# Performance work log

Hardware: AMD Instinct MI355X
Metric: run time of the kernel (lower is better)

## Reference

```python
import jax, jax.numpy as jnp
from jax import lax
import numpy as np

B, T, F, H = 1024, 512, 1, 60


def _p(key, shape, scale):
    return jax.random.uniform(key, shape, jnp.float32, -scale, scale)


def setup_inputs() -> dict:
    key = jax.random.key(0)
    ks = jax.random.split(key, 40)
    s = 1.0 / np.sqrt(H)
    d = {
        "inputs": jax.random.normal(ks[0], (B, T, F), jnp.float32),
        "outputs": jax.random.normal(ks[1], (B, T, F), jnp.float32),
        # encoder GRU: 3 layers, PyTorch layout W_ih [3H, in], W_hh [3H, H]
        "eW_ih0": _p(ks[2], (3 * H, F), s), "eW_hh0": _p(ks[3], (3 * H, H), s),
        "eb_ih0": _p(ks[4], (3 * H,), s), "eb_hh0": _p(ks[5], (3 * H,), s),
        "eW_ih1": _p(ks[6], (3 * H, H), s), "eW_hh1": _p(ks[7], (3 * H, H), s),
        "eb_ih1": _p(ks[8], (3 * H,), s), "eb_hh1": _p(ks[9], (3 * H,), s),
        "eW_ih2": _p(ks[10], (3 * H, H), s), "eW_hh2": _p(ks[11], (3 * H, H), s),
        "eb_ih2": _p(ks[12], (3 * H,), s), "eb_hh2": _p(ks[13], (3 * H,), s),
        # decoder GRUCells
        "c1_Wih": _p(ks[14], (3 * H, F), s), "c1_Whh": _p(ks[15], (3 * H, H), s),
        "c1_bih": _p(ks[16], (3 * H,), s), "c1_bhh": _p(ks[17], (3 * H,), s),
        "c2_Wih": _p(ks[18], (3 * H, H), s), "c2_Whh": _p(ks[19], (3 * H, H), s),
        "c2_bih": _p(ks[20], (3 * H,), s), "c2_bhh": _p(ks[21], (3 * H,), s),
        "c3_Wih": _p(ks[22], (3 * H, H), s), "c3_Whh": _p(ks[23], (3 * H, H), s),
        "c3_bih": _p(ks[24], (3 * H,), s), "c3_bhh": _p(ks[25], (3 * H,), s),
        # output linear
        "lin_W": _p(ks[26], (F, H), s), "lin_b": _p(ks[27], (F,), s),
    }
    return d


def gru_step(x, h, Wih, Whh, bih, bhh):
    # PyTorch GRU gate math
    gi = x @ Wih.T + bih  # [B, 3H]
    gh = h @ Whh.T + bhh
    ir, iz, inn = jnp.split(gi, 3, axis=-1)
    hr, hz, hn = jnp.split(gh, 3, axis=-1)
    r = jax.nn.sigmoid(ir + hr)
    z = jax.nn.sigmoid(iz + hz)
    n = jnp.tanh(inn + r * hn)
    return (1.0 - z) * n + z * h


def run_gru_layer(x_tbf, Wih, Whh, bih, bhh):
    h0 = jnp.zeros((x_tbf.shape[1], H), x_tbf.dtype)

    def step(h, xt):
        h2 = gru_step(xt, h, Wih, Whh, bih, bhh)
        return h2, h2

    hT, ys = lax.scan(step, h0, x_tbf)
    return ys, hT


def reference(inputs, outputs,
              eW_ih0, eW_hh0, eb_ih0, eb_hh0,
              eW_ih1, eW_hh1, eb_ih1, eb_hh1,
              eW_ih2, eW_hh2, eb_ih2, eb_hh2,
              c1_Wih, c1_Whh, c1_bih, c1_bhh,
              c2_Wih, c2_Whh, c2_bih, c2_bhh,
              c3_Wih, c3_Whh, c3_bih, c3_bhh,
              lin_W, lin_b):
    # --- encoder: 3-layer GRU (eval mode -> inter-layer dropout is identity)
    x = jnp.swapaxes(inputs, 0, 1)  # [T, B, F]
    ys0, h0T = run_gru_layer(x, eW_ih0, eW_hh0, eb_ih0, eb_hh0)
    ys1, h1T = run_gru_layer(ys0, eW_ih1, eW_hh1, eb_ih1, eb_hh1)
    _, h2T = run_gru_layer(ys1, eW_ih2, eW_hh2, eb_ih2, eb_hh2)
    encoded_vec = jnp.stack([h0T, h1T, h2T])  # [3, B, H]

    # --- decoder: 3 stacked GRUCells per step (dropout identity in eval)
    outs_r = jnp.swapaxes(outputs, 0, 1)  # [T, B, F]
    carry0 = (encoded_vec[2], encoded_vec[1], encoded_vec[0])

    def dec_step(carry, xt):
        h1, h2, h3 = carry
        h1 = gru_step(xt, h1, c1_Wih, c1_Whh, c1_bih, c1_bhh)
        h2 = gru_step(h1, h2, c2_Wih, c2_Whh, c2_bih, c2_bhh)
        h3 = gru_step(h2, h3, c3_Wih, c3_Whh, c3_bih, c3_bhh)
        pred = h3 @ lin_W.T + lin_b  # [B, F]
        return (h1, h2, h3), pred

    _, preds = lax.scan(dec_step, carry0, outs_r)  # [T, B, F]
    predicted = jnp.swapaxes(preds, 0, 1)  # [B, T, F]
    return predicted, jnp.swapaxes(encoded_vec, 0, 1)  # [B, 3, H]
```

## Files before the change

### kernel.cpp

```cpp
#include <hip/hip_runtime.h>
#include <hip/hip_bf16.h>

namespace {

constexpr int B = 1024, T = 512, H = 60, G = 180, NTHR = 192;
constexpr int TT = 8;
constexpr int NT = T / TT;

__device__ __forceinline__ float sigm(float x) { return 1.f / (1.f + __expf(-x)); }
__device__ __forceinline__ float tanh_fast(float x) {
  x = fminf(fmaxf(x, -15.f), 15.f);
  const float e = __expf(-2.f * x);
  return (1.f - e) / (1.f + e);
}

__device__ __forceinline__ float ldcvt(const float* p) { return *p; }
__device__ __forceinline__ float ldcvt(const __hip_bfloat16* p) { return __bfloat162float(*p); }
__device__ __forceinline__ void stcvt(float* p, float v) { *p = v; }
__device__ __forceinline__ void stcvt(__hip_bfloat16* p, float v) { *p = __float2bfloat16(v); }

#define ACCH(i, dst)                                                  \
  {                                                                   \
    const float4 hv = *(const float4*)&h_sh[(i) * 4];                 \
    dst = fmaf(Wh##i.x, hv.x, dst);                                   \
    dst = fmaf(Wh##i.y, hv.y, dst);                                   \
    dst = fmaf(Wh##i.z, hv.z, dst);                                   \
    dst = fmaf(Wh##i.w, hv.w, dst);                                   \
  }
#define ACCH_ALL                                                      \
  ACCH(0, c0) ACCH(1, c1) ACCH(2, c2) ACCH(3, c3)                     \
  ACCH(4, c0) ACCH(5, c1) ACCH(6, c2) ACCH(7, c3)                     \
  ACCH(8, c0) ACCH(9, c1) ACCH(10, c2) ACCH(11, c3)                   \
  ACCH(12, c0) ACCH(13, c1) ACCH(14, c2)

#define LWH_ALL                                                       \
  LWH(0) LWH(1) LWH(2) LWH(3) LWH(4) LWH(5) LWH(6) LWH(7)             \
  LWH(8) LWH(9) LWH(10) LWH(11) LWH(12) LWH(13) LWH(14)

template <typename TS, bool WRITE_YS, bool WRITE_ENC>
__global__ __launch_bounds__(NTHR, 1) void gru_scalar_kernel(
    const float* __restrict__ xscalar,
    const float* __restrict__ Wih,
    const float* __restrict__ Whh,
    const float* __restrict__ bih, const float* __restrict__ bhh,
    const float* __restrict__ h_init,
    TS* __restrict__ ys_out,
    float* __restrict__ enc_out)
{
  const int tid = threadIdx.x;
  const int b = blockIdx.x;

  __shared__ __align__(16) float h_sh[64];
  __shared__ float Ar[60], Az[60], Nn[60], Hn[60];
  __shared__ float xs_seq[T];

  const int rr = (tid < G) ? tid : 0;

  float4 Wh0, Wh1, Wh2, Wh3, Wh4, Wh5, Wh6, Wh7, Wh8, Wh9, Wh10, Wh11, Wh12, Wh13, Wh14;
#define LWH(i) Wh##i = *(const float4*)&Whh[(size_t)rr * H + (i) * 4];
  LWH_ALL
#undef LWH
  const float wih0 = Wih[rr];
  const float bi = bih[rr];
  const float bh = bhh[rr];

  if (tid < H) h_sh[tid] = h_init ? h_init[(size_t)b * G + tid] : 0.f;
  for (int i = tid; i < T; i += NTHR) xs_seq[i] = xscalar[(size_t)b * T + i];
  __syncthreads();

  const int g = tid / H;
  const int j = tid - g * H;

  for (int t = 0; t < T; ++t) {
    if (tid < G) {
      float c0 = bh, c1 = 0.f, c2 = 0.f, c3 = 0.f;
      ACCH_ALL
      const float c = (c0 + c1) + (c2 + c3);
      const float a = fmaf(wih0, xs_seq[t], bi);
      if (g == 0)       Ar[j] = a + c;
      else if (g == 1)  Az[j] = a + c;
      else            { Nn[j] = a; Hn[j] = c; }
    }
    __syncthreads();

    if (tid < H) {
      const float rg = sigm(Ar[tid]);
      const float zg = sigm(Az[tid]);
      const float nv = tanh_fast(fmaf(rg, Hn[tid], Nn[tid]));
      const float hnew = fmaf(zg, h_sh[tid] - nv, nv);
      h_sh[tid] = hnew;
      if constexpr (WRITE_YS)
        stcvt(&ys_out[(size_t)t * B * H + (size_t)b * H + tid], hnew);
    }
    __syncthreads();
  }

  if constexpr (WRITE_ENC) {
    if (tid < H) enc_out[(size_t)b * G + tid] = h_sh[tid];
  }
}

template <typename TS, bool WRITE_YS, bool WRITE_ENC, bool WRITE_PRED>
__global__ __launch_bounds__(NTHR, 1) void gru_vec_kernel(
    const TS* __restrict__ xseq,
    const float* __restrict__ Wih,
    const float* __restrict__ Whh,
    const float* __restrict__ bih, const float* __restrict__ bhh,
    const float* __restrict__ h_init,
    TS* __restrict__ ys_out,
    float* __restrict__ enc_out,
    float* __restrict__ pred_out,
    const float* __restrict__ lin_W,
    const float* __restrict__ lin_b)
{
  const int tid = threadIdx.x;
  const int b = blockIdx.x;

  __shared__ __align__(16) float h_sh[64];
  __shared__ __align__(16) float x_sh[2][TT * H];
  __shared__ float gi_sh[TT][G];
  __shared__ float Ar[60], Az[60], Nn[60], Hn[60];
  __shared__ float pv[64];

  const int rr = (tid < G) ? tid : 0;

  float4 Wh0, Wh1, Wh2, Wh3, Wh4, Wh5, Wh6, Wh7, Wh8, Wh9, Wh10, Wh11, Wh12, Wh13, Wh14;
#define LWH(i) Wh##i = *(const float4*)&Whh[(size_t)rr * H + (i) * 4];
  LWH_ALL
#undef LWH
  const float bi = bih[rr];
  const float bh = bhh[rr];

  float linw = 0.f, linb = 0.f;
  if constexpr (WRITE_PRED) {
    linw = lin_W[tid < H ? tid : 0];
    linb = lin_b[0];
  }

  if (tid < H) h_sh[tid] = h_init ? h_init[(size_t)b * G + tid] : 0.f;

  {
    const int i0 = tid, i1 = tid + NTHR, i2 = tid + 2 * NTHR;
    {
      const int s = i0 / H, hh = i0 - s * H;
      x_sh[0][i0] = ldcvt(&xseq[((size_t)s * B + b) * H + hh]);
    }
    {
      const int s = i1 / H, hh = i1 - s * H;
      x_sh[0][i1] = ldcvt(&xseq[((size_t)s * B + b) * H + hh]);
    }
    if (i2 < TT * H) {
      const int s = i2 / H, hh = i2 - s * H;
      x_sh[0][i2] = ldcvt(&xseq[((size_t)s * B + b) * H + hh]);
    }
  }
  __syncthreads();

  const int g = tid / H;
  const int j = tid - g * H;

  for (int tile = 0; tile < NT; ++tile) {
    const int cur = tile & 1;

    float xr0 = 0.f, xr1 = 0.f, xr2 = 0.f;
    const int i0 = tid, i1 = tid + NTHR, i2 = tid + 2 * NTHR;
    if (tile + 1 < NT) {
      const size_t tb = (size_t)(tile + 1) * TT;
      {
        const int s = i0 / H, hh = i0 - s * H;
        xr0 = ldcvt(&xseq[((tb + s) * B + b) * H + hh]);
      }
      {
        const int s = i1 / H, hh = i1 - s * H;
        xr1 = ldcvt(&xseq[((tb + s) * B + b) * H + hh]);
      }
      if (i2 < TT * H) {
        const int s = i2 / H, hh = i2 - s * H;
        xr2 = ldcvt(&xseq[((tb + s) * B + b) * H + hh]);
      }
    }

    asm volatile("" ::: "memory");

    if (tid < G) {
      float acc[TT];
#pragma unroll
      for (int s = 0; s < TT; ++s) acc[s] = bi;
#pragma unroll
      for (int k = 0; k < H / 4; ++k) {
        const float4 w = *(const float4*)&Wih[(size_t)rr * H + k * 4];
#pragma unroll
        for (int s = 0; s < TT; ++s) {
          const float4 xv = *(const float4*)&x_sh[cur][s * H + k * 4];
          acc[s] = fmaf(w.x, xv.x, acc[s]);
          acc[s] = fmaf(w.y, xv.y, acc[s]);
          acc[s] = fmaf(w.z, xv.z, acc[s]);
          acc[s] = fmaf(w.w, xv.w, acc[s]);
        }
      }
#pragma unroll
      for (int s = 0; s < TT; ++s) gi_sh[s][rr] = acc[s];
    }

    if (tile + 1 < NT) {
      x_sh[cur ^ 1][i0] = xr0;
      x_sh[cur ^ 1][i1] = xr1;
      if (i2 < TT * H) x_sh[cur ^ 1][i2] = xr2;
    }
    __syncthreads();

    for (int s = 0; s < TT; ++s) {
      const int t = tile * TT + s;
      if (tid < G) {
        float c0 = bh, c1 = 0.f, c2 = 0.f, c3 = 0.f;
        ACCH_ALL
        const float c = (c0 + c1) + (c2 + c3);
        const float a = gi_sh[s][rr];
        if (g == 0)       Ar[j] = a + c;
        else if (g == 1)  Az[j] = a + c;
        else            { Nn[j] = a; Hn[j] = c; }
      }
      __syncthreads();

      if (tid < H) {
        const float rg = sigm(Ar[tid]);
        const float zg = sigm(Az[tid]);
        const float nv = tanh_fast(fmaf(rg, Hn[tid], Nn[tid]));
        const float hnew = fmaf(zg, h_sh[tid] - nv, nv);
        h_sh[tid] = hnew;
        if constexpr (WRITE_YS)
          stcvt(&ys_out[(size_t)t * B * H + (size_t)b * H + tid], hnew);
        if constexpr (WRITE_PRED) pv[tid] = hnew * linw;
      }
      __syncthreads();

      if constexpr (WRITE_PRED) {
        if (tid < 64) {
          float v = (tid < H) ? pv[tid] : 0.f;
#pragma unroll
          for (int off = 32; off; off >>= 1) v += __shfl_xor(v, off);
          if (tid == 0) pred_out[(size_t)b * T + t] = v + linb;
        }
      }
    }
  }

  if constexpr (WRITE_ENC) {
    if (tid < H) enc_out[(size_t)b * G + tid] = h_sh[tid];
  }
}

template <typename TS>
void launch_all(const float* inputs, const float* outputs,
                const float* eW_ih0, const float* eW_hh0, const float* eb_ih0, const float* eb_hh0,
                const float* eW_ih1, const float* eW_hh1, const float* eb_ih1, const float* eb_hh1,
                const float* eW_ih2, const float* eW_hh2, const float* eb_ih2, const float* eb_hh2,
                const float* c1_Wih, const float* c1_Whh, const float* c1_bih, const float* c1_bhh,
                const float* c2_Wih, const float* c2_Whh, const float* c2_bih, const float* c2_bhh,
                const float* c3_Wih, const float* c3_Whh, const float* c3_bih, const float* c3_bhh,
                const float* lin_W, const float* lin_b,
                float* pred, float* enc, void* d_ws, hipStream_t stream) {
  const size_t seq = (size_t)T * B * H;
  TS* ws0 = (TS*)d_ws;
  TS* ws1 = ws0 + seq;
  const dim3 grid(B), blk(NTHR);

  gru_scalar_kernel<TS, true, true><<<grid, blk, 0, stream>>>(
      inputs, eW_ih0, eW_hh0, eb_ih0, eb_hh0, nullptr, ws0, enc + 0);
  gru_vec_kernel<TS, true, true, false><<<grid, blk, 0, stream>>>(
      ws0, eW_ih1, eW_hh1, eb_ih1, eb_hh1, nullptr,
      ws1, enc + 60, nullptr, nullptr, nullptr);
  gru_vec_kernel<TS, false, true, false><<<grid, blk, 0, stream>>>(
      ws1, eW_ih2, eW_hh2, eb_ih2, eb_hh2, nullptr,
      nullptr, enc + 120, nullptr, nullptr, nullptr);
  gru_scalar_kernel<TS, true, false><<<grid, blk, 0, stream>>>(
      outputs, c1_Wih, c1_Whh, c1_bih, c1_bhh, enc + 120, ws0, nullptr);
  gru_vec_kernel<TS, true, false, false><<<grid, blk, 0, stream>>>(
      ws0, c2_Wih, c2_Whh, c2_bih, c2_bhh, enc + 60,
      ws1, nullptr, nullptr, nullptr, nullptr);
  gru_vec_kernel<TS, false, false, true><<<grid, blk, 0, stream>>>(
      ws1, c3_Wih, c3_Whh, c3_bih, c3_bhh, enc + 0,
      nullptr, nullptr, pred, lin_W, lin_b);
}

}

extern "C" void kernel_launch(void* const* d_in, const int* in_sizes, int n_in,
                              void* d_out, int out_size, void* d_ws, size_t ws_size,
                              hipStream_t stream) {
  const float* inputs  = (const float*)d_in[0];
  const float* outputs = (const float*)d_in[1];
  const float* eW_ih0 = (const float*)d_in[2];  const float* eW_hh0 = (const float*)d_in[3];
  const float* eb_ih0 = (const float*)d_in[4];  const float* eb_hh0 = (const float*)d_in[5];
  const float* eW_ih1 = (const float*)d_in[6];  const float* eW_hh1 = (const float*)d_in[7];
  const float* eb_ih1 = (const float*)d_in[8];  const float* eb_hh1 = (const float*)d_in[9];
  const float* eW_ih2 = (const float*)d_in[10]; const float* eW_hh2 = (const float*)d_in[11];
  const float* eb_ih2 = (const float*)d_in[12]; const float* eb_hh2 = (const float*)d_in[13];
  const float* c1_Wih = (const float*)d_in[14]; const float* c1_Whh = (const float*)d_in[15];
  const float* c1_bih = (const float*)d_in[16]; const float* c1_bhh = (const float*)d_in[17];
  const float* c2_Wih = (const float*)d_in[18]; const float* c2_Whh = (const float*)d_in[19];
  const float* c2_bih = (const float*)d_in[20]; const float* c2_bhh = (const float*)d_in[21];
  const float* c3_Wih = (const float*)d_in[22]; const float* c3_Whh = (const float*)d_in[23];
  const float* c3_bih = (const float*)d_in[24]; const float* c3_bhh = (const float*)d_in[25];
  const float* lin_W  = (const float*)d_in[26]; const float* lin_b  = (const float*)d_in[27];

  float* pred = (float*)d_out;
  float* enc  = pred + (size_t)B * T;

  const size_t seq = (size_t)T * B * H;

#define ARGS inputs, outputs, \
    eW_ih0, eW_hh0, eb_ih0, eb_hh0, eW_ih1, eW_hh1, eb_ih1, eb_hh1, \
    eW_ih2, eW_hh2, eb_ih2, eb_hh2, \
    c1_Wih, c1_Whh, c1_bih, c1_bhh, c2_Wih, c2_Whh, c2_bih, c2_bhh, \
    c3_Wih, c3_Whh, c3_bih, c3_bhh, lin_W, lin_b, pred, enc, d_ws, stream

  if (ws_size >= 2 * seq * sizeof(float)) {
    launch_all<float>(ARGS);
  } else {
    launch_all<__hip_bfloat16>(ARGS);
  }
#undef ARGS
}
```

Measured before the change: 3.467 ms.

## Split input projection into separate GEMM kernel, chunk recurrence over time

The input-to-hidden projection for the vector GRU layers moves out of the recurrent kernel into a standalone gi_gemm kernel that computes gate pre-activations for a chunk of timesteps. The recurrent kernel then only does the hidden matvec and prefetches precomputed gi values four steps ahead. The sequence is processed in chunks sized to the workspace. The bf16 fallback is dropped and ys is overwritten in place. The aim is to take the Wih matvec off the serial critical path, at the cost of extra global traffic for gi and more kernel launches.

```diff
diff --git a/kernel.cpp b/kernel.cpp
--- a/kernel.cpp
+++ b/kernel.cpp
@@ -4,8 +4,6 @@
 namespace {
 
 constexpr int B = 1024, T = 512, H = 60, G = 180, NTHR = 192;
-constexpr int TT = 8;
-constexpr int NT = T / TT;
 
 __device__ __forceinline__ float sigm(float x) { return 1.f / (1.f + __expf(-x)); }
 __device__ __forceinline__ float tanh_fast(float x) {
@@ -13,11 +11,6 @@
   const float e = __expf(-2.f * x);
   return (1.f - e) / (1.f + e);
 }
-
-__device__ __forceinline__ float ldcvt(const float* p) { return *p; }
-__device__ __forceinline__ float ldcvt(const __hip_bfloat16* p) { return __bfloat162float(*p); }
-__device__ __forceinline__ void stcvt(float* p, float v) { *p = v; }
-__device__ __forceinline__ void stcvt(__hip_bfloat16* p, float v) { *p = __float2bfloat16(v); }
 
 #define ACCH(i, dst)                                                  \
   {                                                                   \
@@ -27,24 +20,15 @@
     dst = fmaf(Wh##i.z, hv.z, dst);                                   \
     dst = fmaf(Wh##i.w, hv.w, dst);                                   \
   }
-#define ACCH_ALL                                                      \
-  ACCH(0, c0) ACCH(1, c1) ACCH(2, c2) ACCH(3, c3)                     \
-  ACCH(4, c0) ACCH(5, c1) ACCH(6, c2) ACCH(7, c3)                     \
-  ACCH(8, c0) ACCH(9, c1) ACCH(10, c2) ACCH(11, c3)                   \
-  ACCH(12, c0) ACCH(13, c1) ACCH(14, c2)
-
-#define LWH_ALL                                                       \
-  LWH(0) LWH(1) LWH(2) LWH(3) LWH(4) LWH(5) LWH(6) LWH(7)             \
-  LWH(8) LWH(9) LWH(10) LWH(11) LWH(12) LWH(13) LWH(14)
-
-template <typename TS, bool WRITE_YS, bool WRITE_ENC>
+
+template <bool WRITE_YS, bool WRITE_ENC>
 __global__ __launch_bounds__(NTHR, 1) void gru_scalar_kernel(
     const float* __restrict__ xscalar,
     const float* __restrict__ Wih,
     const float* __restrict__ Whh,
     const float* __restrict__ bih, const float* __restrict__ bhh,
     const float* __restrict__ h_init,
-    TS* __restrict__ ys_out,
+    float* __restrict__ ys_out,
     float* __restrict__ enc_out)
 {
   const int tid = threadIdx.x;
@@ -58,13 +42,15 @@
 
   float4 Wh0, Wh1, Wh2, Wh3, Wh4, Wh5, Wh6, Wh7, Wh8, Wh9, Wh10, Wh11, Wh12, Wh13, Wh14;
 #define LWH(i) Wh##i = *(const float4*)&Whh[(size_t)rr * H + (i) * 4];
-  LWH_ALL
+  LWH(0) LWH(1) LWH(2) LWH(3) LWH(4) LWH(5) LWH(6) LWH(7)
+  LWH(8) LWH(9) LWH(10) LWH(11) LWH(12) LWH(13) LWH(14)
 #undef LWH
   const float wih0 = Wih[rr];
   const float bi = bih[rr];
   const float bh = bhh[rr];
 
   if (tid < H) h_sh[tid] = h_init ? h_init[(size_t)b * G + tid] : 0.f;
+  if (tid >= H && tid < 64) h_sh[tid] = 0.f;
   for (int i = tid; i < T; i += NTHR) xs_seq[i] = xscalar[(size_t)b * T + i];
   __syncthreads();
 
@@ -74,7 +60,10 @@
   for (int t = 0; t < T; ++t) {
     if (tid < G) {
       float c0 = bh, c1 = 0.f, c2 = 0.f, c3 = 0.f;
-      ACCH_ALL
+      ACCH(0, c0) ACCH(1, c1) ACCH(2, c2) ACCH(3, c3)
+      ACCH(4, c0) ACCH(5, c1) ACCH(6, c2) ACCH(7, c3)
+      ACCH(8, c0) ACCH(9, c1) ACCH(10, c2) ACCH(11, c3)
+      ACCH(12, c0) ACCH(13, c1) ACCH(14, c2)
       const float c = (c0 + c1) + (c2 + c3);
       const float a = fmaf(wih0, xs_seq[t], bi);
       if (g == 0)       Ar[j] = a + c;
@@ -90,7 +79,7 @@
       const float hnew = fmaf(zg, h_sh[tid] - nv, nv);
       h_sh[tid] = hnew;
       if constexpr (WRITE_YS)
-        stcvt(&ys_out[(size_t)t * B * H + (size_t)b * H + tid], hnew);
+        ys_out[(size_t)t * B * H + (size_t)b * H + tid] = hnew;
     }
     __syncthreads();
   }
@@ -100,25 +89,88 @@
   }
 }
 
-template <typename TS, bool WRITE_YS, bool WRITE_ENC, bool WRITE_PRED>
-__global__ __launch_bounds__(NTHR, 1) void gru_vec_kernel(
-    const TS* __restrict__ xseq,
+__global__ __launch_bounds__(NTHR, 1) void gi_gemm_kernel(
+    const float* __restrict__ x,
     const float* __restrict__ Wih,
-    const float* __restrict__ Whh,
-    const float* __restrict__ bih, const float* __restrict__ bhh,
-    const float* __restrict__ h_init,
-    TS* __restrict__ ys_out,
+    const float* __restrict__ bih,
+    float* __restrict__ gi)
+{
+  __shared__ __align__(16) float xs[16 * 60];
+  const int tid = threadIdx.x;
+  const size_t row0 = (size_t)blockIdx.x * 16;
+  const int rr = (tid < G) ? tid : 0;
+
+  float4 W0, W1, W2, W3, W4, W5, W6, W7, W8, W9, W10, W11, W12, W13, W14;
+#define LW(i) W##i = *(const float4*)&Wih[(size_t)rr * H + (i) * 4];
+  LW(0) LW(1) LW(2) LW(3) LW(4) LW(5) LW(6) LW(7)
+  LW(8) LW(9) LW(10) LW(11) LW(12) LW(13) LW(14)
+#undef LW
+  const float bi = bih[rr];
+
+  {
+    const float4* s4 = (const float4*)(x + row0 * H);
+    float4* d4 = (float4*)xs;
+    d4[tid] = s4[tid];
+    const int i2 = tid + NTHR;
+    if (i2 < 240) d4[i2] = s4[i2];
+  }
+  __syncthreads();
+
+#define GX(s, a)                                                      \
+  {                                                                   \
+    const float4 xv = *(const float4*)&xb[(s) * H + 4 * kk];          \
+    a = fmaf(w.x, xv.x, a); a = fmaf(w.y, xv.y, a);                   \
+    a = fmaf(w.z, xv.z, a); a = fmaf(w.w, xv.w, a);                   \
+  }
+#define PASS(p)                                                       \
+  {                                                                   \
+    const float* xb = xs + (p) * 8 * H;                               \
+    float a0 = bi, a1 = bi, a2 = bi, a3 = bi;                         \
+    float a4 = bi, a5 = bi, a6 = bi, a7 = bi;                         \
+    _Pragma("unroll")                                                 \
+    for (int kk = 0; kk < 15; ++kk) {                                 \
+      float4 w;                                                       \
+      switch (kk) {                                                   \
+        case 0: w = W0; break;   case 1: w = W1; break;               \
+        case 2: w = W2; break;   case 3: w = W3; break;               \
+        case 4: w = W4; break;   case 5: w = W5; break;               \
+        case 6: w = W6; break;   case 7: w = W7; break;               \
+        case 8: w = W8; break;   case 9: w = W9; break;               \
+        case 10: w = W10; break; case 11: w = W11; break;             \
+        case 12: w = W12; break; case 13: w = W13; break;             \
+        default: w = W14; break;                                      \
+      }                                                               \
+      GX(0, a0) GX(1, a1) GX(2, a2) GX(3, a3)                         \
+      GX(4, a4) GX(5, a5) GX(6, a6) GX(7, a7)                         \
+    }                                                                 \
+    if (tid < G) {                                                    \
+      float* o = gi + (row0 + (p) * 8) * G + rr;                      \
+      o[0 * G] = a0; o[1 * G] = a1; o[2 * G] = a2; o[3 * G] = a3;     \
+      o[4 * G] = a4; o[5 * G] = a5; o[6 * G] = a6; o[7 * G] = a7;     \
+    }                                                                 \
+  }
+  PASS(0)
+  PASS(1)
+#undef PASS
+#undef GX
+}
+
+template <bool WRITE_YS, bool WRITE_PRED>
+__global__ __launch_bounds__(NTHR, 1) void gru_rec_kernel(
+    const float* __restrict__ gi,
+    const float* __restrict__ Whh, const float* __restrict__ bhh,
+    const float* __restrict__ h_in, int h_in_stride,
+    float* __restrict__ ys_out,
+    float* __restrict__ h_out,
     float* __restrict__ enc_out,
     float* __restrict__ pred_out,
-    const float* __restrict__ lin_W,
-    const float* __restrict__ lin_b)
+    const float* __restrict__ linW, const float* __restrict__ linb,
+    int t0, int nsteps)
 {
   const int tid = threadIdx.x;
   const int b = blockIdx.x;
 
   __shared__ __align__(16) float h_sh[64];
-  __shared__ __align__(16) float x_sh[2][TT * H];
-  __shared__ float gi_sh[TT][G];
   __shared__ float Ar[60], Az[60], Nn[60], Hn[60];
   __shared__ float pv[64];
 
@@ -126,161 +178,100 @@
 
   float4 Wh0, Wh1, Wh2, Wh3, Wh4, Wh5, Wh6, Wh7, Wh8, Wh9, Wh10, Wh11, Wh12, Wh13, Wh14;
 #define LWH(i) Wh##i = *(const float4*)&Whh[(size_t)rr * H + (i) * 4];
-  LWH_ALL
+  LWH(0) LWH(1) LWH(2) LWH(3) LWH(4) LWH(5) LWH(6) LWH(7)
+  LWH(8) LWH(9) LWH(10) LWH(11) LWH(12) LWH(13) LWH(14)
 #undef LWH
-  const float bi = bih[rr];
   const float bh = bhh[rr];
 
-  float linw = 0.f, linb = 0.f;
+  float linw = 0.f, lb = 0.f;
   if constexpr (WRITE_PRED) {
-    linw = lin_W[tid < H ? tid : 0];
-    linb = lin_b[0];
-  }
-
-  if (tid < H) h_sh[tid] = h_init ? h_init[(size_t)b * G + tid] : 0.f;
-
-  {
-    const int i0 = tid, i1 = tid + NTHR, i2 = tid + 2 * NTHR;
-    {
-      const int s = i0 / H, hh = i0 - s * H;
-      x_sh[0][i0] = ldcvt(&xseq[((size_t)s * B + b) * H + hh]);
-    }
-    {
-      const int s = i1 / H, hh = i1 - s * H;
-      x_sh[0][i1] = ldcvt(&xseq[((size_t)s * B + b) * H + hh]);
-    }
-    if (i2 < TT * H) {
-      const int s = i2 / H, hh = i2 - s * H;
-      x_sh[0][i2] = ldcvt(&xseq[((size_t)s * B + b) * H + hh]);
-    }
-  }
+    linw = linW[tid < H ? tid : 0];
+    lb = linb[0];
+  }
+
+  if (tid < H) h_sh[tid] = h_in ? h_in[(size_t)b * h_in_stride + tid] : 0.f;
+  if (tid >= H && tid < 64) h_sh[tid] = 0.f;
   __syncthreads();
 
-  const int g = tid / H;
-  const int j = tid - g * H;
-
-  for (int tile = 0; tile < NT; ++tile) {
-    const int cur = tile & 1;
-
-    float xr0 = 0.f, xr1 = 0.f, xr2 = 0.f;
-    const int i0 = tid, i1 = tid + NTHR, i2 = tid + 2 * NTHR;
-    if (tile + 1 < NT) {
-      const size_t tb = (size_t)(tile + 1) * TT;
-      {
-        const int s = i0 / H, hh = i0 - s * H;
-        xr0 = ldcvt(&xseq[((tb + s) * B + b) * H + hh]);
+  const int g = rr / H;
+  const int j = rr - g * H;
+  const bool rowact = tid < G;
+
+  float g0 = 0.f, g1 = 0.f, g2 = 0.f, g3 = 0.f;
+  if (rowact) {
+    g0 = gi[((size_t)0 * B + b) * G + rr];
+    g1 = gi[((size_t)1 * B + b) * G + rr];
+    g2 = gi[((size_t)2 * B + b) * G + rr];
+    g3 = gi[((size_t)3 * B + b) * G + rr];
+  }
+
+  for (int s = 0; s < nsteps; ++s) {
+    float gn = 0.f;
+    if (rowact && s + 4 < nsteps) gn = gi[((size_t)(s + 4) * B + b) * G + rr];
+
+    if (rowact) {
+      float c0 = bh, c1 = 0.f, c2 = 0.f, c3 = 0.f;
+      ACCH(0, c0) ACCH(1, c1) ACCH(2, c2) ACCH(3, c3)
+      ACCH(4, c0) ACCH(5, c1) ACCH(6, c2) ACCH(7, c3)
+      ACCH(8, c0) ACCH(9, c1) ACCH(10, c2) ACCH(11, c3)
+      ACCH(12, c0) ACCH(13, c1) ACCH(14, c2)
+      const float c = (c0 + c1) + (c2 + c3);
+      const float a = g0;
+      if (g == 0)       Ar[j] = a + c;
+      else if (g == 1)  Az[j] = a + c;
+      else            { Nn[j] = a; Hn[j] = c; }
+    }
+    g0 = g1; g1 = g2; g2 = g3; g3 = gn;
+    __syncthreads();
+
+    if (tid < H) {
+      const float rg = sigm(Ar[tid]);
+      const float zg = sigm(Az[tid]);
+      const float nv = tanh_fast(fmaf(rg, Hn[tid], Nn[tid]));
+      const float hnew = fmaf(zg, h_sh[tid] - nv, nv);
+      h_sh[tid] = hnew;
+      if constexpr (WRITE_YS)
+        ys_out[(size_t)s * B * H + (size_t)b * H + tid] = hnew;
+      if constexpr (WRITE_PRED) pv[tid] = hnew * linw;
+    }
+    __syncthreads();
+
+    if constexpr (WRITE_PRED) {
+      if (tid < 64) {
+        float v = (tid < H) ? pv[tid] : 0.f;
+#pragma unroll
+        for (int o = 32; o; o >>= 1) v += __shfl_xor(v, o);
+        if (tid == 0) pred_out[(size_t)b * T + t0 + s] = v + lb;
       }
-      {
-        const int s = i1 / H, hh = i1 - s * H;
-        xr1 = ldcvt(&xseq[((tb + s) * B + b) * H + hh]);
-      }
-      if (i2 < TT * H) {
-        const int s = i2 / H, hh = i2 - s * H;
-        xr2 = ldcvt(&xseq[((tb + s) * B + b) * H + hh]);
-      }
-    }
-
-    asm volatile("" ::: "memory");
-
-    if (tid < G) {
-      float acc[TT];
-#pragma unroll
-      for (int s = 0; s < TT; ++s) acc[s] = bi;
-#pragma unroll
-      for (int k = 0; k < H / 4; ++k) {
-        const float4 w = *(const float4*)&Wih[(size_t)rr * H + k * 4];
-#pragma unroll
-        for (int s = 0; s < TT; ++s) {
-          const float4 xv = *(const float4*)&x_sh[cur][s * H + k * 4];
-          acc[s] = fmaf(w.x, xv.x, acc[s]);
-          acc[s] = fmaf(w.y, xv.y, acc[s]);
-          acc[s] = fmaf(w.z, xv.z, acc[s]);
-          acc[s] = fmaf(w.w, xv.w, acc[s]);
-        }
-      }
-#pragma unroll
-      for (int s = 0; s < TT; ++s) gi_sh[s][rr] = acc[s];
-    }
-
-    if (tile + 1 < NT) {
-      x_sh[cur ^ 1][i0] = xr0;
-      x_sh[cur ^ 1][i1] = xr1;
-      if (i2 < TT * H) x_sh[cur ^ 1][i2] = xr2;
-    }
-    __syncthreads();
-
-    for (int s = 0; s < TT; ++s) {
-      const int t = tile * TT + s;
-      if (tid < G) {
-        float c0 = bh, c1 = 0.f, c2 = 0.f, c3 = 0.f;
-        ACCH_ALL
-        const float c = (c0 + c1) + (c2 + c3);
-        const float a = gi_sh[s][rr];
-        if (g == 0)       Ar[j] = a + c;
-        else if (g == 1)  Az[j] = a + c;
-        else            { Nn[j] = a; Hn[j] = c; }
-      }
-      __syncthreads();
-
-      if (tid < H) {
-        const float rg = sigm(Ar[tid]);
-        const float zg = sigm(Az[tid]);
-        const float nv = tanh_fast(fmaf(rg, Hn[tid], Nn[tid]));
-        const float hnew = fmaf(zg, h_sh[tid] - nv, nv);
-        h_sh[tid] = hnew;
-        if constexpr (WRITE_YS)
-          stcvt(&ys_out[(size_t)t * B * H + (size_t)b * H + tid], hnew);
-        if constexpr (WRITE_PRED) pv[tid] = hnew * linw;
-      }
-      __syncthreads();
-
-      if constexpr (WRITE_PRED) {
-        if (tid < 64) {
-          float v = (tid < H) ? pv[tid] : 0.f;
-#pragma unroll
-          for (int off = 32; off; off >>= 1) v += __shfl_xor(v, off);
-          if (tid == 0) pred_out[(size_t)b * T + t] = v + linb;
-        }
-      }
-    }
-  }
-
-  if constexpr (WRITE_ENC) {
-    if (tid < H) enc_out[(size_t)b * G + tid] = h_sh[tid];
-  }
-}
-
-template <typename TS>
-void launch_all(const float* inputs, const float* outputs,
-                const float* eW_ih0, const float* eW_hh0, const float* eb_ih0, const float* eb_hh0,
-                const float* eW_ih1, const float* eW_hh1, const float* eb_ih1, const float* eb_hh1,
-                const float* eW_ih2, const float* eW_hh2, const float* eb_ih2, const float* eb_hh2,
-                const float* c1_Wih, const float* c1_Whh, const float* c1_bih, const float* c1_bhh,
-                const float* c2_Wih, const float* c2_Whh, const float* c2_bih, const float* c2_bhh,
-                const float* c3_Wih, const float* c3_Whh, const float* c3_bih, const float* c3_bhh,
-                const float* lin_W, const float* lin_b,
-                float* pred, float* enc, void* d_ws, hipStream_t stream) {
-  const size_t seq = (size_t)T * B * H;
-  TS* ws0 = (TS*)d_ws;
-  TS* ws1 = ws0 + seq;
-  const dim3 grid(B), blk(NTHR);
-
-  gru_scalar_kernel<TS, true, true><<<grid, blk, 0, stream>>>(
-      inputs, eW_ih0, eW_hh0, eb_ih0, eb_hh0, nullptr, ws0, enc + 0);
-  gru_vec_kernel<TS, true, true, false><<<grid, blk, 0, stream>>>(
-      ws0, eW_ih1, eW_hh1, eb_ih1, eb_hh1, nullptr,
-      ws1, enc + 60, nullptr, nullptr, nullptr);
-  gru_vec_kernel<TS, false, true, false><<<grid, blk, 0, stream>>>(
-      ws1, eW_ih2, eW_hh2, eb_ih2, eb_hh2, nullptr,
-      nullptr, enc + 120, nullptr, nullptr, nullptr);
-  gru_scalar_kernel<TS, true, false><<<grid, blk, 0, stream>>>(
-      outputs, c1_Wih, c1_Whh, c1_bih, c1_bhh, enc + 120, ws0, nullptr);
-  gru_vec_kernel<TS, true, false, false><<<grid, blk, 0, stream>>>(
-      ws0, c2_Wih, c2_Whh, c2_bih, c2_bhh, enc + 60,
-      ws1, nullptr, nullptr, nullptr, nullptr);
-  gru_vec_kernel<TS, false, false, true><<<grid, blk, 0, stream>>>(
-      ws1, c3_Wih, c3_Whh, c3_bih, c3_bhh, enc + 0,
-      nullptr, nullptr, pred, lin_W, lin_b);
+    }
+  }
+
+  if (tid < H) {
+    h_out[(size_t)b * H + tid] = h_sh[tid];
+    if (enc_out) enc_out[(size_t)b * G + tid] = h_sh[tid];
+  }
+}
+
+template <bool WRITE_YS, bool WRITE_PRED>
+void run_vec_layer(const float* Wih, const float* bih,
+                   const float* Whh, const float* bhh,
+                   const float* h_init_slot,
+                   float* enc_slot_out,
+                   float* ysA, float* gic, float* hio,
+                   float* pred, const float* linW, const float* linb,
+                   int nch, hipStream_t stream) {
+  const int tn = T / nch;
+  for (int c = 0; c < nch; ++c) {
+    const int t0 = c * tn;
+    gi_gemm_kernel<<<dim3((tn * B) / 16), dim3(NTHR), 0, stream>>>(
+        ysA + (size_t)t0 * B * H, Wih, bih, gic);
+    gru_rec_kernel<WRITE_YS, WRITE_PRED><<<dim3(B), dim3(NTHR), 0, stream>>>(
+        gic, Whh, bhh,
+        c ? hio : h_init_slot, c ? H : G,
+        ysA + (size_t)t0 * B * H, hio,
+        (c == nch - 1) ? enc_slot_out : nullptr,
+        pred, linW, linb, t0, tn);
+  }
 }
 
 }
@@ -309,16 +300,27 @@
 
   const size_t seq = (size_t)T * B * H;
 
-#define ARGS inputs, outputs, \
-    eW_ih0, eW_hh0, eb_ih0, eb_hh0, eW_ih1, eW_hh1, eb_ih1, eb_hh1, \
-    eW_ih2, eW_hh2, eb_ih2, eb_hh2, \
-    c1_Wih, c1_Whh, c1_bih, c1_bhh, c2_Wih, c2_Whh, c2_bih, c2_bhh, \
-    c3_Wih, c3_Whh, c3_bih, c3_bhh, lin_W, lin_b, pred, enc, d_ws, stream
-
-  if (ws_size >= 2 * seq * sizeof(float)) {
-    launch_all<float>(ARGS);
-  } else {
-    launch_all<__hip_bfloat16>(ARGS);
-  }
-#undef ARGS
-}
+  int nch = 64;
+  for (int c : {1, 2, 4, 8, 16, 32}) {
+    const size_t need = seq * 4 + (size_t)(T / c) * B * G * 4 + (size_t)B * H * 4;
+    if (ws_size >= need) { nch = c; break; }
+  }
+
+  float* ysA = (float*)d_ws;
+  float* gic = ysA + seq;
+  float* hio = gic + (size_t)(T / nch) * B * G;
+
+  gru_scalar_kernel<true, true><<<dim3(B), dim3(NTHR), 0, stream>>>(
+      inputs, eW_ih0, eW_hh0, eb_ih0, eb_hh0, nullptr, ysA, enc + 0);
+  run_vec_layer<true, false>(eW_ih1, eb_ih1, eW_hh1, eb_hh1, nullptr, enc + 60,
+                             ysA, gic, hio, pred, lin_W, lin_b, nch, stream);
+  run_vec_layer<false, false>(eW_ih2, eb_ih2, eW_hh2, eb_hh2, nullptr, enc + 120,
+                              ysA, gic, hio, pred, lin_W, lin_b, nch, stream);
+
+  gru_scalar_kernel<true, false><<<dim3(B), dim3(NTHR), 0, stream>>>(
+      outputs, c1_Wih, c1_Whh, c1_bih, c1_bhh, enc + 120, ysA, nullptr);
+  run_vec_layer<true, false>(c2_Wih, c2_bih, c2_Whh, c2_bhh, enc + 60, nullptr,
+                             ysA, gic, hio, pred, lin_W, lin_b, nch, stream);
+  run_vec_layer<false, true>(c3_Wih, c3_bih, c3_Whh, c3_bhh, enc + 0, nullptr,
+                             ysA, gic, hio, pred, lin_W, lin_b, nch, stream);
+}
```

New measurement: 3.324 ms. 1.04x faster.
